# Kernel tuning notes

Hardware: AMD Instinct MI355X
Metric: run time of the kernel (lower is better)

Reference implementation:

```python
import jax, jax.numpy as jnp
import numpy as np

B, C, H, W = 64, 256, 32, 32
K, D = 1024, 256
COMMIT = 0.25
DECAY = 0.99
EPS = 1e-05


def setup_inputs() -> dict:
    key = jax.random.key(0)
    k1, k2, k3 = jax.random.split(key, 3)
    return {
        "inputs": jax.random.normal(k1, (B, C, H, W), dtype=jnp.float32),
        "embedding": jax.random.normal(k2, (K, D), dtype=jnp.float32),
        "ema_cluster_size": jnp.zeros((K,), dtype=jnp.float32),
        "ema_w": jax.random.normal(k3, (K, D), dtype=jnp.float32),
    }


def reference(inputs, embedding, ema_cluster_size, ema_w):
    # NCHW -> NHWC, flatten to [N, D]
    x = jnp.transpose(inputs, (0, 2, 3, 1))  # [B,H,W,D]
    in_shape = x.shape
    flat = x.reshape(-1, D)  # [N, D]

    dist = (jnp.sum(flat * flat, axis=1, keepdims=True)
            + jnp.sum(embedding * embedding, axis=1)
            - 2.0 * jnp.matmul(flat, embedding.T))
    idx = jnp.argmin(dist, axis=1)  # [N] int
    encodings = jax.nn.one_hot(idx, K, dtype=flat.dtype)  # [N, K]

    quantized = jnp.matmul(encodings, embedding).reshape(in_shape)  # [B,H,W,D]

    # EMA updates (training branch)
    cluster = ema_cluster_size * DECAY + (1.0 - DECAY) * jnp.sum(encodings, axis=0)
    n = jnp.sum(cluster)
    cluster = (cluster + EPS) / (n + K * EPS) * n
    dw = jnp.matmul(encodings.T, flat)  # [K, D]
    new_ema_w = ema_w * DECAY + (1.0 - DECAY) * dw
    new_embedding = new_ema_w / cluster[:, None]

    # commitment loss (quantized detached)
    e_latent_loss = jnp.mean((jax.lax.stop_gradient(quantized) - x) ** 2)
    loss = COMMIT * e_latent_loss

    # straight-through estimator
    quantized_st = x + jax.lax.stop_gradient(quantized - x)

    avg_probs = jnp.mean(encodings, axis=0)
    vq_entropy = -jnp.sum(avg_probs * jnp.log(avg_probs + 1e-10))

    out = jnp.transpose(quantized_st, (0, 3, 1, 2))  # back to NCHW
    return out, loss, vq_entropy, encodings, cluster, new_ema_w, new_embedding
```

## Files before the change

### kernel.cpp

```cpp
#include <hip/hip_runtime.h>

#define B_    64
#define C_    256
#define H_    32
#define W_    32
#define K_    1024
#define D_    256
#define HW_   1024
#define N_    65536
#define NELEM 16777216
#define DECAY_ 0.99f
#define OMD_   0.01f
#define EPS_   1e-5f
#define TAU_   0.05f

#define OFF_LOSS    16777216
#define OFF_ENT     16777217
#define OFF_ENC     16777218
#define OFF_CLUSTER 83886082
#define OFF_NEWW    83887106
#define OFF_NEWEMB  84149250

#define OFF_XHI     (OFF_ENC + 2)
#define OFF_XLO     (OFF_XHI + 8388608)
#define OFF_EHI     (OFF_XLO + 8388608)
#define OFF_ELO     (OFF_EHI + 131072)
#define OFF_SORT2   (OFF_ELO + 131072)
#define ZTAIL_ABS   33884168
#define ZTAIL_F4    12500478
#define ZHEAD_F4    4276737

typedef __attribute__((ext_vector_type(8)))  short short8;
typedef __attribute__((ext_vector_type(16))) float floatx16;

__device__ __forceinline__ unsigned short f2bf(float f) {
    unsigned u = __float_as_uint(f);
    return (unsigned short)((u + 0x7fffu + ((u >> 16) & 1u)) >> 16);
}
__device__ __forceinline__ float bf2f(unsigned short h) {
    return __uint_as_float(((unsigned)h) << 16);
}

__global__ __launch_bounds__(256) void k_zero(float* __restrict__ dw, int* __restrict__ small_) {
    int g = blockIdx.x * 256 + threadIdx.x;
    dw[g] = 0.0f;
    if (g < 1026) small_[g] = 0;
}

__global__ __launch_bounds__(64) void k_prep_e(const float* __restrict__ emb,
                                               unsigned short* __restrict__ ehi,
                                               unsigned short* __restrict__ elo,
                                               float* __restrict__ enorm) {
    const int k = blockIdx.x;
    const int t = threadIdx.x;
    float4 v = ((const float4*)(emb + (size_t)k * D_))[t];
    float s = v.x * v.x + v.y * v.y + v.z * v.z + v.w * v.w;
    ushort4 hi, lo;
    {
        float f[4] = {v.x, v.y, v.z, v.w};
        unsigned short h[4], l[4];
        #pragma unroll
        for (int j = 0; j < 4; ++j) {
            h[j] = f2bf(f[j]);
            l[j] = f2bf(f[j] - bf2f(h[j]));
        }
        hi = make_ushort4(h[0], h[1], h[2], h[3]);
        lo = make_ushort4(l[0], l[1], l[2], l[3]);
    }
    size_t o = ((size_t)(k >> 5) << 13) + ((size_t)(t >> 2) << 9)
             + (((size_t)(t >> 1) & 1) << 8) + ((size_t)(k & 31) << 3) + ((t & 1) << 2);
    *(ushort4*)(ehi + o) = hi;
    *(ushort4*)(elo + o) = lo;
    #pragma unroll
    for (int off = 32; off > 0; off >>= 1) s += __shfl_down(s, off);
    if (t == 0) enorm[k] = s;
}

__global__ __launch_bounds__(256) void k_prep_x(const float* __restrict__ inp,
                                                unsigned short* __restrict__ xhi,
                                                unsigned short* __restrict__ xlo) {
    __shared__ float tile[32][257];
    const int tid = threadIdx.x;
    const int bid = blockIdx.x;
    const int dt = bid & 7;
    const int ht = (bid >> 3) & 3;
    const int b = bid >> 5;
    const int d0 = dt * 32;
    const int hw0 = ht * 256;
    const float* src = inp + (size_t)b * (C_ * HW_) + (size_t)d0 * HW_ + hw0;
    #pragma unroll
    for (int i = 0; i < 8; ++i) {
        int idx4 = i * 256 + tid;
        int dl = idx4 >> 6;
        int nl4 = (idx4 & 63) * 4;
        float4 v = *(const float4*)(src + (size_t)dl * HW_ + nl4);
        tile[dl][nl4] = v.x; tile[dl][nl4 + 1] = v.y;
        tile[dl][nl4 + 2] = v.z; tile[dl][nl4 + 3] = v.w;
    }
    __syncthreads();
    const int nbase = b * HW_ + hw0;
    #pragma unroll
    for (int i = 0; i < 4; ++i) {
        int f8 = i * 256 + tid;
        int nl = f8 >> 2;
        int dpos = (f8 & 3) * 8;
        union { unsigned short u[8]; short8 v; } ph, pl;
        #pragma unroll
        for (int j = 0; j < 8; ++j) {
            float f = -2.0f * tile[dpos + j][nl];
            unsigned short h = f2bf(f);
            ph.u[j] = h;
            pl.u[j] = f2bf(f - bf2f(h));
        }
        size_t o = (size_t)(nbase + nl) * D_ + d0 + dpos;
        *(short8*)(xhi + o) = ph.v;
        *(short8*)(xlo + o) = pl.v;
    }
}

__device__ __forceinline__ void stage_tile(const unsigned short* __restrict__ gh,
                                           const unsigned short* __restrict__ gl,
                                           unsigned short* sh, unsigned short* sl,
                                           int tid) {
    #pragma unroll
    for (int i = 0; i < 4; ++i) {
        __builtin_amdgcn_global_load_lds(
            (const __attribute__((address_space(1))) unsigned int*)(gh + i * 2048 + tid * 8),
            (__attribute__((address_space(3))) unsigned int*)(sh + i * 2048 + tid * 8),
            16, 0, 0);
        __builtin_amdgcn_global_load_lds(
            (const __attribute__((address_space(1))) unsigned int*)(gl + i * 2048 + tid * 8),
            (__attribute__((address_space(3))) unsigned int*)(sl + i * 2048 + tid * 8),
            16, 0, 0);
    }
}

__global__ __launch_bounds__(256, 2) void k_argmin(
    const unsigned short* __restrict__ xhi, const unsigned short* __restrict__ xlo,
    const unsigned short* __restrict__ ehi, const unsigned short* __restrict__ elo,
    const float* __restrict__ enorm, int* __restrict__ idx_out,
    int* __restrict__ flagcount, int* __restrict__ flaglist,
    float4* __restrict__ encz)
{
    __shared__ unsigned short smem[2][2][8192];
    const int tid = threadIdx.x;
    const int w = tid >> 6;
    const int lane = tid & 63;
    const int c32 = lane & 31;
    const int h = lane >> 5;
    const int r0 = blockIdx.x * 128 + w * 32;
    const int gtid = blockIdx.x * 256 + tid;
    const float4 z4 = make_float4(0.f, 0.f, 0.f, 0.f);

    short8 Ahi[16], Alo[16];
    {
        const unsigned short* pa = xhi + (size_t)(r0 + c32) * D_ + h * 8;
        const unsigned short* pl = xlo + (size_t)(r0 + c32) * D_ + h * 8;
        #pragma unroll
        for (int ds = 0; ds < 16; ++ds) {
            Ahi[ds] = *(const short8*)(pa + ds * 16);
            Alo[ds] = *(const short8*)(pl + ds * 16);
        }
    }

    float b1[16], b2[16];
    int bi[16];
    #pragma unroll
    for (int i = 0; i < 16; ++i) { b1[i] = 3.0e38f; b2[i] = 3.0e38f; bi[i] = 0; }

    stage_tile(ehi, elo, &smem[0][0][0], &smem[0][1][0], tid);
    __syncthreads();

    const int rb = (h << 8) + (c32 << 3);

    int cb = 0;
    for (int ct = 0; ct < 32; ++ct) {
        if (ct + 1 < 32) {
            stage_tile(ehi + (size_t)(ct + 1) * 8192, elo + (size_t)(ct + 1) * 8192,
                       &smem[cb ^ 1][0][0], &smem[cb ^ 1][1][0], tid);
        }
        __builtin_amdgcn_sched_barrier(0);
        #pragma unroll
        for (int jj = 0; jj < 3; ++jj) {
            int zi = (ct * 3 + jj) * 131072 + gtid;
            zi = (zi < ZTAIL_F4) ? zi : (ZTAIL_F4 - 1);
            encz[zi] = z4;
        }
        const int col = ct * 32 + c32;
        const float en = enorm[col];
        const unsigned short* sbh = &smem[cb][0][rb];
        const unsigned short* sbl = &smem[cb][1][rb];
        floatx16 hh, cr;
        #pragma unroll
        for (int i = 0; i < 16; ++i) { hh[i] = 0.0f; cr[i] = 0.0f; }
        #pragma unroll
        for (int ds = 0; ds < 16; ++ds) {
            short8 bh = *(const short8*)(sbh + ds * 512);
            short8 bl = *(const short8*)(sbl + ds * 512);
            hh = __builtin_amdgcn_mfma_f32_32x32x16_bf16(Ahi[ds], bh, hh, 0, 0, 0);
            cr = __builtin_amdgcn_mfma_f32_32x32x16_bf16(Ahi[ds], bl, cr, 0, 0, 0);
            cr = __builtin_amdgcn_mfma_f32_32x32x16_bf16(Alo[ds], bh, cr, 0, 0, 0);
        }
        #pragma unroll
        for (int r = 0; r < 16; ++r) {
            float v = hh[r] + cr[r] + en;
            bool lt = v < b1[r];
            float nb2 = lt ? b1[r] : fminf(v, b2[r]);
            b2[r] = nb2;
            b1[r] = lt ? v : b1[r];
            bi[r] = lt ? col : bi[r];
        }
        asm volatile("s_waitcnt vmcnt(3)" ::: "memory");
        __builtin_amdgcn_sched_barrier(0);
        __builtin_amdgcn_s_barrier();
        __builtin_amdgcn_sched_barrier(0);
        cb ^= 1;
    }

    #pragma unroll
    for (int r = 0; r < 16; ++r) {
        float B1 = b1[r], B2 = b2[r];
        int Bi = bi[r];
        #pragma unroll
        for (int mask = 1; mask <= 16; mask <<= 1) {
            float v1 = __shfl_xor(B1, mask);
            float v2 = __shfl_xor(B2, mask);
            int i1 = __shfl_xor(Bi, mask);
            if (v1 < B1 || (v1 == B1 && i1 < Bi)) {
                B2 = fminf(fminf(B1, B2), v2);
                B1 = v1; Bi = i1;
            } else {
                B2 = fminf(B2, fminf(v1, v2));
            }
        }
        if (c32 == 0) {
            int row = r0 + (r & 3) + 4 * h + 8 * (r >> 2);
            idx_out[row] = Bi;
            if (B2 - B1 < TAU_) {
                int p = atomicAdd(flagcount, 1);
                flaglist[p] = row;
            }
        }
    }
}

__global__ __launch_bounds__(256) void k_rescan(
    const float* __restrict__ inp, const float* __restrict__ emb,
    const int* __restrict__ flagcount, const int* __restrict__ flaglist,
    int* __restrict__ idx_out)
{
    __shared__ double xd[256];
    __shared__ double sv[256];
    __shared__ int si[256];
    const int tid = threadIdx.x;
    const int nflag = *flagcount;
    for (int f = blockIdx.x; f < nflag; f += gridDim.x) {
        int n = flaglist[f];
        int b = n >> 10, nn = n & 1023;
        xd[tid] = (double)inp[(size_t)b * (C_ * HW_) + (size_t)tid * HW_ + nn];
        __syncthreads();
        double bv = 1e300; int bi = 0;
        for (int k = tid; k < K_; k += 256) {
            const float* ep = emb + (size_t)k * D_;
            double dot = 0.0, en = 0.0;
            for (int d = 0; d < D_; ++d) {
                double e = (double)ep[d];
                dot = fma(xd[d], e, dot);
                en  = fma(e, e, en);
            }
            double v = en - 2.0 * dot;
            if (v < bv) { bv = v; bi = k; }
        }
        sv[tid] = bv; si[tid] = bi;
        __syncthreads();
        for (int s = 128; s > 0; s >>= 1) {
            if (tid < s) {
                if (sv[tid + s] < sv[tid] || (sv[tid + s] == sv[tid] && si[tid + s] < si[tid])) {
                    sv[tid] = sv[tid + s]; si[tid] = si[tid + s];
                }
            }
            __syncthreads();
        }
        if (tid == 0) idx_out[n] = si[0];
        __syncthreads();
    }
}

__global__ __launch_bounds__(256) void k_hist(const int* __restrict__ idx, int* __restrict__ counts) {
    __shared__ int h[1024];
    const int tid = threadIdx.x;
    #pragma unroll
    for (int j = 0; j < 4; ++j) h[tid + j * 256] = 0;
    __syncthreads();
    #pragma unroll
    for (int j = 0; j < 4; ++j) {
        int n = blockIdx.x * 1024 + j * 256 + tid;
        atomicAdd(&h[idx[n]], 1);
    }
    __syncthreads();
    #pragma unroll
    for (int j = 0; j < 4; ++j) {
        int v = h[tid + j * 256];
        if (v) atomicAdd(&counts[tid + j * 256], v);
    }
}

__global__ __launch_bounds__(1024) void k_scan(const int* __restrict__ counts,
                                               int* __restrict__ offsets, int* __restrict__ cursor) {
    __shared__ int s[1024];
    const int t = threadIdx.x;
    const int c = counts[t];
    s[t] = c;
    __syncthreads();
    for (int off = 1; off < 1024; off <<= 1) {
        int v = (t >= off) ? s[t - off] : 0;
        __syncthreads();
        s[t] += v;
        __syncthreads();
    }
    int excl = s[t] - c;
    offsets[t] = excl;
    cursor[t] = excl;
    if (t == 1023) offsets[1024] = s[1023];
}

__global__ __launch_bounds__(256) void k_scatter(const int* __restrict__ idx,
                                                 int* __restrict__ cursor, int* __restrict__ sorted) {
    __shared__ int hc[1024];
    __shared__ int hb[1024];
    const int tid = threadIdx.x;
    const int base = blockIdx.x * 1024;
    #pragma unroll
    for (int j = 0; j < 4; ++j) hc[tid + j * 256] = 0;
    __syncthreads();
    int myk[4], myn[4];
    #pragma unroll
    for (int j = 0; j < 4; ++j) {
        int n = base + j * 256 + tid;
        myn[j] = n;
        myk[j] = idx[n];
        atomicAdd(&hc[myk[j]], 1);
    }
    __syncthreads();
    #pragma unroll
    for (int j = 0; j < 4; ++j) {
        int kk = tid + j * 256;
        int c = hc[kk];
        hb[kk] = c ? atomicAdd(&cursor[kk], c) : 0;
    }
    __syncthreads();
    #pragma unroll
    for (int j = 0; j < 4; ++j) hc[tid + j * 256] = 0;
    __syncthreads();
    #pragma unroll
    for (int j = 0; j < 4; ++j) {
        int p = hb[myk[j]] + atomicAdd(&hc[myk[j]], 1);
        sorted[p] = myn[j];
    }
}

__global__ __launch_bounds__(256) void k_dwg(const unsigned short* __restrict__ xhi,
                                             const unsigned short* __restrict__ xlo,
                                             const int* __restrict__ sorted,
                                             const int* __restrict__ idx,
                                             const int* __restrict__ offsets,
                                             float* __restrict__ dw) {
    const int lane = threadIdx.x & 63;
    const int wid = threadIdx.x >> 6;
    const int wbase = (blockIdx.x * 4 + wid) * 64;

    int myn = sorted[wbase + lane];
    int myk = idx[myn];

    float4 acc = make_float4(0.f, 0.f, 0.f, 0.f);
    int cur = __shfl(myk, 0);

    #pragma unroll 8
    for (int i = 0; i < 64; ++i) {
        int n = __shfl(myn, i);
        int k = __shfl(myk, i);
        if (k != cur) {
            bool full = (offsets[cur] >= wbase) && (offsets[cur + 1] <= wbase + 64);
            float* dwk = dw + (size_t)cur * D_ + lane * 4;
            if (full) {
                ((float2*)dwk)[0] = make_float2(-0.5f * acc.x, -0.5f * acc.y);
                ((float2*)dwk)[1] = make_float2(-0.5f * acc.z, -0.5f * acc.w);
            } else {
                atomicAdd(dwk + 0, -0.5f * acc.x);
                atomicAdd(dwk + 1, -0.5f * acc.y);
                atomicAdd(dwk + 2, -0.5f * acc.z);
                atomicAdd(dwk + 3, -0.5f * acc.w);
            }
            acc = make_float4(0.f, 0.f, 0.f, 0.f);
            cur = k;
        }
        size_t o = (size_t)n * D_ + lane * 4;
        ushort4 hx = *(const ushort4*)(xhi + o);
        ushort4 lx = *(const ushort4*)(xlo + o);
        acc.x += bf2f(hx.x) + bf2f(lx.x);
        acc.y += bf2f(hx.y) + bf2f(lx.y);
        acc.z += bf2f(hx.z) + bf2f(lx.z);
        acc.w += bf2f(hx.w) + bf2f(lx.w);
    }
    {
        bool full = (offsets[cur] >= wbase) && (offsets[cur + 1] <= wbase + 64);
        float* dwk = dw + (size_t)cur * D_ + lane * 4;
        if (full) {
            ((float2*)dwk)[0] = make_float2(-0.5f * acc.x, -0.5f * acc.y);
            ((float2*)dwk)[1] = make_float2(-0.5f * acc.z, -0.5f * acc.w);
        } else {
            atomicAdd(dwk + 0, -0.5f * acc.x);
            atomicAdd(dwk + 1, -0.5f * acc.y);
            atomicAdd(dwk + 2, -0.5f * acc.z);
            atomicAdd(dwk + 3, -0.5f * acc.w);
        }
    }
}

__global__ __launch_bounds__(256) void k_enc0(float* __restrict__ enc) {
    const float4 z = make_float4(0.f, 0.f, 0.f, 0.f);
    float4* p = (float4*)(enc + 2);
    int t = blockIdx.x * 256 + threadIdx.x;
    #pragma unroll
    for (int it = 0; it < 5; ++it) {
        int i = it * 1048576 + t;
        if (i < ZHEAD_F4) p[i] = z;
    }
    if (t == 0) { enc[0] = 0.f; enc[1] = 0.f; enc[67108862] = 0.f; enc[67108863] = 0.f; }
}

__global__ __launch_bounds__(256) void k_enc1(const int* __restrict__ idx, float* __restrict__ enc) {
    #pragma unroll
    for (int j = 0; j < 4; ++j) {
        int n = blockIdx.x * 1024 + j * 256 + threadIdx.x;
        enc[(size_t)n * 1024 + idx[n]] = 1.0f;
    }
}

__global__ __launch_bounds__(256) void k_quant(
    const float* __restrict__ inp, const float* __restrict__ emb,
    const int* __restrict__ idx, float* __restrict__ outp, float* __restrict__ losssum)
{
    __shared__ float red[256];
    const int tid = threadIdx.x;
    float s = 0.0f;
    const int base = blockIdx.x * 1024;
    #pragma unroll
    for (int it = 0; it < 4; ++it) {
        int g = base + it * 256 + tid;
        int o = g << 2;
        int b = o >> 18;
        int c = (o >> 10) & 255;
        int hw = o & 1023;
        int n = (b << 10) + hw;
        float4 x = ((const float4*)inp)[g];
        int4 ki = *(const int4*)(idx + n);
        float q0 = emb[(size_t)ki.x * D_ + c];
        float q1 = emb[(size_t)ki.y * D_ + c];
        float q2 = emb[(size_t)ki.z * D_ + c];
        float q3 = emb[(size_t)ki.w * D_ + c];
        float d0 = q0 - x.x, d1 = q1 - x.y, d2 = q2 - x.z, d3 = q3 - x.w;
        ((float4*)outp)[g] = make_float4(x.x + d0, x.y + d1, x.z + d2, x.w + d3);
        s += d0 * d0 + d1 * d1 + d2 * d2 + d3 * d3;
    }
    red[tid] = s;
    __syncthreads();
    for (int t = 128; t > 0; t >>= 1) {
        if (tid < t) red[tid] += red[tid + t];
        __syncthreads();
    }
    if (tid == 0) atomicAdd(losssum, red[0]);
}

__global__ __launch_bounds__(1024) void k_cluster(
    const float* __restrict__ ema_cs, const int* __restrict__ counts,
    const float* __restrict__ losssum, float* __restrict__ out_cluster,
    float* __restrict__ out_loss, float* __restrict__ out_ent)
{
    __shared__ float red[1024];
    const int k = threadIdx.x;
    float cnt = (float)counts[k];
    float raw = ema_cs[k] * DECAY_ + OMD_ * cnt;
    red[k] = raw;
    __syncthreads();
    for (int t = 512; t > 0; t >>= 1) {
        if (k < t) red[k] += red[k + t];
        __syncthreads();
    }
    float nsum = red[0];
    __syncthreads();
    float clv = (raw + EPS_) / (nsum + 1024.0f * EPS_) * nsum;
    out_cluster[k] = clv;
    float p = cnt * (1.0f / 65536.0f);
    red[k] = p * logf(p + 1e-10f);
    __syncthreads();
    for (int t = 512; t > 0; t >>= 1) {
        if (k < t) red[k] += red[k + t];
        __syncthreads();
    }
    if (k == 0) {
        out_ent[0] = -red[0];
        out_loss[0] = 0.25f * losssum[0] * (1.0f / 16777216.0f);
    }
}

__global__ __launch_bounds__(256) void k_fin(
    const float* __restrict__ ema_w, const float* __restrict__ cluster,
    float* __restrict__ neww, float* __restrict__ newemb)
{
    int g = blockIdx.x * 256 + threadIdx.x;
    int k = g >> 8;
    float w = ema_w[g] * DECAY_ + OMD_ * neww[g];
    neww[g] = w;
    newemb[g] = w / cluster[k];
}

extern "C" void kernel_launch(void* const* d_in, const int* in_sizes, int n_in,
                              void* d_out, int out_size, void* d_ws, size_t ws_size,
                              hipStream_t stream)
{
    const float* inp    = (const float*)d_in[0];
    const float* emb    = (const float*)d_in[1];
    const float* ema_cs = (const float*)d_in[2];
    const float* ema_w  = (const float*)d_in[3];

    float* out0        = (float*)d_out;
    float* out_loss    = out0 + OFF_LOSS;
    float* out_ent     = out0 + OFF_ENT;
    float* out_enc     = out0 + OFF_ENC;
    float* out_cluster = out0 + OFF_CLUSTER;
    float* out_neww    = out0 + OFF_NEWW;
    float* out_newemb  = out0 + OFF_NEWEMB;

    unsigned short* ws_xhi  = (unsigned short*)(out0 + OFF_XHI);
    unsigned short* ws_xlo  = (unsigned short*)(out0 + OFF_XLO);
    unsigned short* ws_ehi  = (unsigned short*)(out0 + OFF_EHI);
    unsigned short* ws_elo  = (unsigned short*)(out0 + OFF_ELO);
    int*   ws_sorted  = (int*)(out0 + OFF_SORT2);
    int*   ws_offsets = ws_sorted + 65536;
    int*   ws_cursor  = ws_offsets + 1025;

    int*   ws_idx    = (int*)d_ws;
    int*   ws_counts = ws_idx + 65536;
    int*   ws_flagc  = ws_idx + 66560;
    float* ws_loss   = (float*)(ws_idx + 66561);
    int*   ws_flagl  = ws_idx + 66562;
    float* ws_enorm  = (float*)(ws_idx + 132098);

    float4* encz = (float4*)(out0 + ZTAIL_ABS);

    k_zero   <<<1024, 256, 0, stream>>>(out_neww, ws_counts);
    k_prep_e <<<1024, 64, 0, stream>>>(emb, ws_ehi, ws_elo, ws_enorm);
    k_prep_x <<<2048, 256, 0, stream>>>(inp, ws_xhi, ws_xlo);
    k_argmin <<<512, 256, 0, stream>>>(ws_xhi, ws_xlo, ws_ehi, ws_elo, ws_enorm,
                                       ws_idx, ws_flagc, ws_flagl, encz);
    k_rescan <<<256, 256, 0, stream>>>(inp, emb, ws_flagc, ws_flagl, ws_idx);
    k_hist   <<<64, 256, 0, stream>>>(ws_idx, ws_counts);
    k_scan   <<<1, 1024, 0, stream>>>(ws_counts, ws_offsets, ws_cursor);
    k_scatter<<<64, 256, 0, stream>>>(ws_idx, ws_cursor, ws_sorted);
    k_dwg    <<<256, 256, 0, stream>>>(ws_xhi, ws_xlo, ws_sorted, ws_idx, ws_offsets, out_neww);
    k_enc0   <<<4096, 256, 0, stream>>>(out_enc);
    k_enc1   <<<64, 256, 0, stream>>>(ws_idx, out_enc);
    k_quant  <<<4096, 256, 0, stream>>>(inp, emb, ws_idx, out0, ws_loss);
    k_cluster<<<1, 1024, 0, stream>>>(ema_cs, ws_counts, ws_loss, out_cluster, out_loss, out_ent);
    k_fin    <<<1024, 256, 0, stream>>>(ema_w, out_cluster, out_neww, out_newemb);
}
```

Measured before the change: 730.2 us.

## Fuse zeroing into prep_x and encoding zero-fill into a shared-memory tiled quantize kernel

Folds the dw/counter zeroing kernel into k_prep_x and the encoding-head zero-fill into the quantize kernel, removing two launches. The quantize kernel is restructured so each block stages 64 selected codebook rows in shared memory and reads them transposed, instead of doing scattered per-element gathers from the embedding table. Each block of the reworked kernel now carries both a large zero-fill store stream and the quantize work, and it uses a 64x260 float LDS tile that may reduce occupancy.

```diff
diff --git a/kernel.cpp b/kernel.cpp
--- a/kernel.cpp
+++ b/kernel.cpp
@@ -41,12 +41,6 @@
     return __uint_as_float(((unsigned)h) << 16);
 }
 
-__global__ __launch_bounds__(256) void k_zero(float* __restrict__ dw, int* __restrict__ small_) {
-    int g = blockIdx.x * 256 + threadIdx.x;
-    dw[g] = 0.0f;
-    if (g < 1026) small_[g] = 0;
-}
-
 __global__ __launch_bounds__(64) void k_prep_e(const float* __restrict__ emb,
                                                unsigned short* __restrict__ ehi,
                                                unsigned short* __restrict__ elo,
@@ -78,10 +72,17 @@
 
 __global__ __launch_bounds__(256) void k_prep_x(const float* __restrict__ inp,
                                                 unsigned short* __restrict__ xhi,
-                                                unsigned short* __restrict__ xlo) {
+                                                unsigned short* __restrict__ xlo,
+                                                float* __restrict__ dw,
+                                                int* __restrict__ small_) {
     __shared__ float tile[32][257];
     const int tid = threadIdx.x;
     const int bid = blockIdx.x;
+    if (bid < 1024) {
+        int g = bid * 256 + tid;
+        dw[g] = 0.0f;
+        if (g < 1026) small_[g] = 0;
+    }
     const int dt = bid & 7;
     const int ht = (bid >> 3) & 3;
     const int b = bid >> 5;
@@ -417,16 +418,68 @@
     }
 }
 
-__global__ __launch_bounds__(256) void k_enc0(float* __restrict__ enc) {
-    const float4 z = make_float4(0.f, 0.f, 0.f, 0.f);
-    float4* p = (float4*)(enc + 2);
-    int t = blockIdx.x * 256 + threadIdx.x;
-    #pragma unroll
-    for (int it = 0; it < 5; ++it) {
-        int i = it * 1048576 + t;
-        if (i < ZHEAD_F4) p[i] = z;
-    }
-    if (t == 0) { enc[0] = 0.f; enc[1] = 0.f; enc[67108862] = 0.f; enc[67108863] = 0.f; }
+__global__ __launch_bounds__(256) void k_quant(
+    const float* __restrict__ inp, const float* __restrict__ emb,
+    const int* __restrict__ idx, float* __restrict__ outp, float* __restrict__ losssum,
+    float* __restrict__ enc)
+{
+    __shared__ float qt[64][260];
+    __shared__ int karr[64];
+    __shared__ float red[256];
+    const int tid = threadIdx.x;
+    const int bid = blockIdx.x;
+    const int b = bid >> 4;
+    const int ht = bid & 15;
+    const int base_n = b * HW_ + ht * 64;
+
+    {
+        const float4 z4 = make_float4(0.f, 0.f, 0.f, 0.f);
+        float4* pz = (float4*)(enc + 2);
+        int t = bid * 256 + tid;
+        #pragma unroll
+        for (int it = 0; it < 17; ++it) {
+            int i = it * 262144 + t;
+            if (i < ZHEAD_F4) pz[i] = z4;
+        }
+        if (t == 0) { enc[0] = 0.f; enc[1] = 0.f; enc[67108862] = 0.f; enc[67108863] = 0.f; }
+    }
+
+    if (tid < 64) karr[tid] = idx[base_n + tid];
+    __syncthreads();
+
+    #pragma unroll
+    for (int it = 0; it < 16; ++it) {
+        int f = it * 256 + tid;
+        int r = f >> 6;
+        int c4 = (f & 63) << 2;
+        float4 v = ((const float4*)emb)[karr[r] * 64 + (c4 >> 2)];
+        *(float4*)(&qt[r][c4]) = v;
+    }
+    __syncthreads();
+
+    float s = 0.0f;
+    #pragma unroll
+    for (int it = 0; it < 16; ++it) {
+        int f = it * 256 + tid;
+        int c = f >> 4;
+        int hl = (f & 15) << 2;
+        int g = b * 65536 + c * 256 + ht * 16 + (hl >> 2);
+        float4 x = ((const float4*)inp)[g];
+        float q0 = qt[hl + 0][c];
+        float q1 = qt[hl + 1][c];
+        float q2 = qt[hl + 2][c];
+        float q3 = qt[hl + 3][c];
+        float d0 = q0 - x.x, d1 = q1 - x.y, d2 = q2 - x.z, d3 = q3 - x.w;
+        ((float4*)outp)[g] = make_float4(x.x + d0, x.y + d1, x.z + d2, x.w + d3);
+        s += d0 * d0 + d1 * d1 + d2 * d2 + d3 * d3;
+    }
+    red[tid] = s;
+    __syncthreads();
+    for (int t = 128; t > 0; t >>= 1) {
+        if (tid < t) red[tid] += red[tid + t];
+        __syncthreads();
+    }
+    if (tid == 0) atomicAdd(losssum, red[0]);
 }
 
 __global__ __launch_bounds__(256) void k_enc1(const int* __restrict__ idx, float* __restrict__ enc) {
@@ -435,41 +488,6 @@
         int n = blockIdx.x * 1024 + j * 256 + threadIdx.x;
         enc[(size_t)n * 1024 + idx[n]] = 1.0f;
     }
-}
-
-__global__ __launch_bounds__(256) void k_quant(
-    const float* __restrict__ inp, const float* __restrict__ emb,
-    const int* __restrict__ idx, float* __restrict__ outp, float* __restrict__ losssum)
-{
-    __shared__ float red[256];
-    const int tid = threadIdx.x;
-    float s = 0.0f;
-    const int base = blockIdx.x * 1024;
-    #pragma unroll
-    for (int it = 0; it < 4; ++it) {
-        int g = base + it * 256 + tid;
-        int o = g << 2;
-        int b = o >> 18;
-        int c = (o >> 10) & 255;
-        int hw = o & 1023;
-        int n = (b << 10) + hw;
-        float4 x = ((const float4*)inp)[g];
-        int4 ki = *(const int4*)(idx + n);
-        float q0 = emb[(size_t)ki.x * D_ + c];
-        float q1 = emb[(size_t)ki.y * D_ + c];
-        float q2 = emb[(size_t)ki.z * D_ + c];
-        float q3 = emb[(size_t)ki.w * D_ + c];
-        float d0 = q0 - x.x, d1 = q1 - x.y, d2 = q2 - x.z, d3 = q3 - x.w;
-        ((float4*)outp)[g] = make_float4(x.x + d0, x.y + d1, x.z + d2, x.w + d3);
-        s += d0 * d0 + d1 * d1 + d2 * d2 + d3 * d3;
-    }
-    red[tid] = s;
-    __syncthreads();
-    for (int t = 128; t > 0; t >>= 1) {
-        if (tid < t) red[tid] += red[tid + t];
-        __syncthreads();
-    }
-    if (tid == 0) atomicAdd(losssum, red[0]);
 }
 
 __global__ __launch_bounds__(1024) void k_cluster(
@@ -549,9 +567,8 @@
 
     float4* encz = (float4*)(out0 + ZTAIL_ABS);
 
-    k_zero   <<<1024, 256, 0, stream>>>(out_neww, ws_counts);
     k_prep_e <<<1024, 64, 0, stream>>>(emb, ws_ehi, ws_elo, ws_enorm);
-    k_prep_x <<<2048, 256, 0, stream>>>(inp, ws_xhi, ws_xlo);
+    k_prep_x <<<2048, 256, 0, stream>>>(inp, ws_xhi, ws_xlo, out_neww, ws_counts);
     k_argmin <<<512, 256, 0, stream>>>(ws_xhi, ws_xlo, ws_ehi, ws_elo, ws_enorm,
                                        ws_idx, ws_flagc, ws_flagl, encz);
     k_rescan <<<256, 256, 0, stream>>>(inp, emb, ws_flagc, ws_flagl, ws_idx);
@@ -559,9 +576,8 @@
     k_scan   <<<1, 1024, 0, stream>>>(ws_counts, ws_offsets, ws_cursor);
     k_scatter<<<64, 256, 0, stream>>>(ws_idx, ws_cursor, ws_sorted);
     k_dwg    <<<256, 256, 0, stream>>>(ws_xhi, ws_xlo, ws_sorted, ws_idx, ws_offsets, out_neww);
-    k_enc0   <<<4096, 256, 0, stream>>>(out_enc);
+    k_quant  <<<1024, 256, 0, stream>>>(inp, emb, ws_idx, out0, ws_loss, out_enc);
     k_enc1   <<<64, 256, 0, stream>>>(ws_idx, out_enc);
-    k_quant  <<<4096, 256, 0, stream>>>(inp, emb, ws_idx, out0, ws_loss);
     k_cluster<<<1, 1024, 0, stream>>>(ema_cs, ws_counts, ws_loss, out_cluster, out_loss, out_ent);
     k_fin    <<<1024, 256, 0, stream>>>(ema_w, out_cluster, out_neww, out_newemb);
 }
```

New measurement: 662.3 us. 9.3% less time.
